# Kernel tuning notes

Measured on AMD Instinct MI355X. Metric: run time of the kernel, lower is better.

## Reference

```python
import jax, jax.numpy as jnp
import numpy as np

K = 256           # number of selected features (init kwarg k)
NUM_SAMPLES = 8   # init kwarg num_samples
BATCH = 256
NUM_FEATURES = 20000


def setup_inputs() -> dict:
    key = jax.random.key(0)
    logits = jax.random.normal(key, (BATCH, NUM_FEATURES, 1), dtype=jnp.float32)
    return {"logits": logits, "tau": 1, "training": 0}


def reference(logits, tau, training):
    # Eval branch of SubsetLayer.forward (training=False).
    # logits: [B, N, 1]
    B, N, _ = logits.shape
    scores = logits[..., 0]                       # [B, N]
    _, idx = jax.lax.top_k(scores, K)             # idx: [B, K]
    # k-hot mask built directly by scatter (equivalent to one_hot(...).sum(1))
    khot = jnp.zeros((B, N), dtype=jnp.float32)
    khot = khot.at[jnp.arange(B)[:, None], idx].set(1.0)  # [B, N]
    # unsqueeze(0).unsqueeze(-1).expand(num_samples, -1, -1, -1)
    out = jnp.broadcast_to(khot[None, :, :, None], (NUM_SAMPLES, B, N, 1))
    return out
```

## Files before the change

### kernel.cpp

```cpp
#include <hip/hip_runtime.h>

#define BATCH   256
#define NFEAT   20000
#define NVEC    (NFEAT / 4)
#define KSEL    256
#define NSAMP   8
#define CAP     2048

typedef unsigned long long u64;
typedef float __attribute__((ext_vector_type(4))) f32x4;

__device__ __forceinline__ unsigned fmap(float f) {
    unsigned u = __float_as_uint(f);
    return (u & 0x80000000u) ? ~u : (u | 0x80000000u);
}

__device__ __forceinline__ void select_bin_wave0(const unsigned* hist, int nbins, int w,
                                                 int* s_d, int* s_w, int lane) {
    for (int base = nbins - 1; base >= 0; base -= 64) {
        int bin = base - lane;
        unsigned c = (bin >= 0) ? hist[bin] : 0u;
        unsigned p = c;
#pragma unroll
        for (int off = 1; off < 64; off <<= 1) {
            unsigned t = __shfl_up(p, off);
            if (lane >= off) p += t;
        }
        unsigned long long m = __ballot(p >= (unsigned)w);
        if (m) {
            int l = __ffsll(m) - 1;
            if (lane == l) { *s_d = bin; *s_w = w - (int)(p - c); }
            return;
        }
        w -= (int)__shfl(p, 63);
    }
    if (lane == 0) { *s_d = 0; *s_w = 1; }
}

__device__ __forceinline__ void pick64(const unsigned* arr, int w, int lane,
                                       int* s_idx, int* s_w) {
    unsigned c = arr[63 - lane];
    unsigned p = c;
#pragma unroll
    for (int off = 1; off < 64; off <<= 1) {
        unsigned t = __shfl_up(p, off);
        if (lane >= off) p += t;
    }
    unsigned long long m = __ballot(p >= (unsigned)w);
    if (m) {
        int l = __ffsll(m) - 1;
        if (lane == l) { *s_idx = 63 - l; *s_w = w - (int)(p - c); }
    } else if (lane == 0) { *s_idx = 0; *s_w = 1; }
}

__global__ __launch_bounds__(1024) void topk_fused(const float* __restrict__ logits,
                                                   float* __restrict__ out) {
    const int b = blockIdx.x, tid = threadIdx.x;
    const int lane = tid & 63, wave = tid >> 6;
    const float4* __restrict__ row4 = (const float4*)(logits + (size_t)b * NFEAT);

    __shared__ unsigned hist[4096];
    __shared__ u64 cand[CAP];
    __shared__ unsigned csum[64];
    __shared__ int s_d, s_w;
    __shared__ unsigned s_cnt;
    __shared__ u64 s_thr;
    __shared__ int s_run, s_cut, s_wc[16];

    float4 v[5];
#pragma unroll
    for (int j = 0; j < 5; ++j) {
        const int i4 = tid + j * 1024;
        v[j] = row4[(i4 < NVEC) ? i4 : (NVEC - 1)];
    }
#pragma unroll
    for (int j = 0; j < 4; ++j) hist[tid + j * 1024] = 0;
    __syncthreads();

    unsigned kk[5][4];
#pragma unroll
    for (int j = 0; j < 5; ++j) {
        kk[j][0] = fmap(v[j].x); kk[j][1] = fmap(v[j].y);
        kk[j][2] = fmap(v[j].z); kk[j][3] = fmap(v[j].w);
    }
#pragma unroll
    for (int j = 0; j < 4; ++j) {
#pragma unroll
        for (int e = 0; e < 4; ++e) atomicAdd(&hist[kk[j][e] >> 20], 1u);
    }
    if (tid + 4096 < NVEC) {
#pragma unroll
        for (int e = 0; e < 4; ++e) atomicAdd(&hist[kk[4][e] >> 20], 1u);
    }
    __syncthreads();

    unsigned keypref; int w;
    {
#pragma unroll
        for (int j = 0; j < 4; ++j) {
            const int c = wave * 4 + j;
            unsigned x = hist[c * 64 + lane];
#pragma unroll
            for (int off = 32; off; off >>= 1) x += __shfl_down(x, off);
            if (lane == 0) csum[c] = x;
        }
        __syncthreads();
        if (wave == 0) pick64(csum, KSEL, lane, &s_d, &s_w);
        __syncthreads();
        const int chunk = s_d; const int w0 = s_w;
        if (wave == 0) pick64(&hist[chunk * 64], w0, lane, &s_d, &s_w);
        if (tid == 0) s_cnt = 0;
        __syncthreads();
        keypref = (unsigned)(chunk * 64 + s_d);
        w = s_w;
    }
    int shift = 20;

    unsigned C;
    for (;;) {
#pragma unroll
        for (int j = 0; j < 5; ++j) {
            const int i4 = tid + j * 1024;
            if (i4 < NVEC) {
#pragma unroll
                for (int e = 0; e < 4; ++e) {
                    const unsigned k = kk[j][e];
                    if ((k >> shift) == keypref) {
                        unsigned p = atomicAdd(&s_cnt, 1u);
                        if (p < CAP) cand[p] = ((u64)k << 32) | (unsigned)~(4 * i4 + e);
                    }
                }
            }
        }
        __syncthreads();
        C = s_cnt;
        if (C <= CAP || shift == 0) break;

        const int nb = (shift >= 12) ? 12 : shift;
        const int nsh = shift - nb;
        for (int i = tid; i < (1 << nb); i += 1024) hist[i] = 0;
        __syncthreads();
#pragma unroll
        for (int j = 0; j < 5; ++j) {
            const int i4 = tid + j * 1024;
            if (i4 < NVEC) {
#pragma unroll
                for (int e = 0; e < 4; ++e) {
                    const unsigned k = kk[j][e];
                    if ((k >> shift) == keypref)
                        atomicAdd(&hist[(k >> nsh) & ((1u << nb) - 1u)], 1u);
                }
            }
        }
        __syncthreads();
        if (wave == 0) select_bin_wave0(hist, 1 << nb, w, &s_d, &s_w, lane);
        if (tid == 0) s_cnt = 0;
        __syncthreads();
        keypref = (keypref << nb) | (unsigned)s_d;
        w = s_w;
        shift = nsh;
    }

    if (C <= CAP) {
        for (int i = tid; i < (int)C; i += 1024) {
            const u64 ci = cand[i];
            int cgt = 0;
            for (int j = 0; j < (int)C; ++j) cgt += (cand[j] > ci) ? 1 : 0;
            if (cgt == w - 1) s_thr = ci;
        }
        __syncthreads();
    } else {
        if (tid == 0) { s_run = 0; s_cut = 0; }
        __syncthreads();
#pragma unroll 1
        for (int j = 0; j < 5; ++j) {
            const int i4 = tid + j * 1024;
            bool eq[4];
            int cnt4 = 0;
#pragma unroll
            for (int e = 0; e < 4; ++e) {
                eq[e] = (i4 < NVEC) && (kk[j][e] == keypref);
                cnt4 += eq[e] ? 1 : 0;
            }
            unsigned p = (unsigned)cnt4;
#pragma unroll
            for (int off = 1; off < 64; off <<= 1) {
                unsigned t = __shfl_up(p, off);
                if (lane >= off) p += t;
            }
            const unsigned excl = p - (unsigned)cnt4;
            if (lane == 63) s_wc[wave] = (int)p;
            __syncthreads();
            int off0 = s_run + (int)excl;
            for (int x = 0; x < wave; ++x) off0 += s_wc[x];
#pragma unroll
            for (int e = 0; e < 4; ++e) {
                if (eq[e]) { if (off0 == w - 1) s_cut = 4 * i4 + e; ++off0; }
            }
            __syncthreads();
            if (tid == 0) { int t = 0; for (int x = 0; x < 16; ++x) t += s_wc[x]; s_run += t; }
            __syncthreads();
            if (s_run >= w) break;
        }
        if (tid == 0) s_thr = ((u64)keypref << 32) | (unsigned)~s_cut;
        __syncthreads();
    }

    const u64 thr = s_thr;
    const unsigned thr_k = (unsigned)(thr >> 32);
    const unsigned thr_l = (unsigned)thr;
    float* const outb = out + (size_t)b * NFEAT;
#pragma unroll
    for (int j = 0; j < 5; ++j) {
        const int i4 = tid + j * 1024;
        if (i4 < NVEC) {
            const int n = 4 * i4;
            f32x4 m;
#pragma unroll
            for (int e = 0; e < 4; ++e) {
                const unsigned k = kk[j][e];
                const bool sel = (k > thr_k) || (k == thr_k && (unsigned)~(n + e) >= thr_l);
                m[e] = sel ? 1.0f : 0.0f;
            }
#pragma unroll
            for (int s = 0; s < NSAMP; ++s) {
                *reinterpret_cast<f32x4*>(outb + (size_t)s * ((size_t)BATCH * NFEAT) + n) = m;
            }
        }
    }
}

extern "C" void kernel_launch(void* const* d_in, const int* in_sizes, int n_in,
                              void* d_out, int out_size, void* d_ws, size_t ws_size,
                              hipStream_t stream) {
    const float* logits = (const float*)d_in[0];
    float* out = (float*)d_out;
    (void)d_ws; (void)ws_size;

    topk_fused<<<BATCH, 1024, 0, stream>>>(logits, out);
}
```

Measured before the change: 36.63 us.

## Overlap zero-fill output stores with top-k selection; write only selected ones

Writes zeros to every output slot early, spread across the histogram and selection phases, so the large output write overlaps the selection compute. At the end it stores 1.0 as scalar writes only for the selected elements, after waiting for the zero stores to finish so the two writes to the same address are ordered. It also replaces __syncthreads with a custom barrier that waits only on LDS counters, so the in-flight global stores do not stall each barrier. The risks are correctness, since ordering relies on the vmcnt wait before the selected-element stores, and scattered scalar stores for the ones.

```diff
diff --git a/kernel.cpp b/kernel.cpp
--- a/kernel.cpp
+++ b/kernel.cpp
@@ -10,6 +10,10 @@
 typedef unsigned long long u64;
 typedef float __attribute__((ext_vector_type(4))) f32x4;
 
+#define BAR() do { asm volatile("s_waitcnt lgkmcnt(0)" ::: "memory"); \
+                   __builtin_amdgcn_s_barrier();                      \
+                   asm volatile("" ::: "memory"); } while (0)
+
 __device__ __forceinline__ unsigned fmap(float f) {
     unsigned u = __float_as_uint(f);
     return (u & 0x80000000u) ? ~u : (u | 0x80000000u);
@@ -58,6 +62,19 @@
     const int b = blockIdx.x, tid = threadIdx.x;
     const int lane = tid & 63, wave = tid >> 6;
     const float4* __restrict__ row4 = (const float4*)(logits + (size_t)b * NFEAT);
+    const size_t BN = (size_t)BATCH * NFEAT;
+    float* const outb = out + (size_t)b * NFEAT;
+    const f32x4 z4 = {0.0f, 0.0f, 0.0f, 0.0f};
+
+#define ZSTORE(J)                                                              \
+    do {                                                                       \
+        const int i4_ = tid + (J) * 1024;                                      \
+        if (i4_ < NVEC) {                                                      \
+            _Pragma("unroll")                                                  \
+            for (int s_ = 0; s_ < NSAMP; ++s_)                                 \
+                *reinterpret_cast<f32x4*>(outb + (size_t)s_ * BN + 4 * i4_) = z4; \
+        }                                                                      \
+    } while (0)
 
     __shared__ unsigned hist[4096];
     __shared__ u64 cand[CAP];
@@ -73,9 +90,11 @@
         const int i4 = tid + j * 1024;
         v[j] = row4[(i4 < NVEC) ? i4 : (NVEC - 1)];
     }
+    ZSTORE(0);
+    ZSTORE(1);
 #pragma unroll
     for (int j = 0; j < 4; ++j) hist[tid + j * 1024] = 0;
-    __syncthreads();
+    BAR();
 
     unsigned kk[5][4];
 #pragma unroll
@@ -92,7 +111,8 @@
 #pragma unroll
         for (int e = 0; e < 4; ++e) atomicAdd(&hist[kk[4][e] >> 20], 1u);
     }
-    __syncthreads();
+    ZSTORE(2);
+    BAR();
 
     unsigned keypref; int w;
     {
@@ -104,17 +124,18 @@
             for (int off = 32; off; off >>= 1) x += __shfl_down(x, off);
             if (lane == 0) csum[c] = x;
         }
-        __syncthreads();
+        BAR();
         if (wave == 0) pick64(csum, KSEL, lane, &s_d, &s_w);
-        __syncthreads();
+        BAR();
         const int chunk = s_d; const int w0 = s_w;
         if (wave == 0) pick64(&hist[chunk * 64], w0, lane, &s_d, &s_w);
         if (tid == 0) s_cnt = 0;
-        __syncthreads();
+        BAR();
         keypref = (unsigned)(chunk * 64 + s_d);
         w = s_w;
     }
     int shift = 20;
+    ZSTORE(3);
 
     unsigned C;
     for (;;) {
@@ -132,14 +153,14 @@
                 }
             }
         }
-        __syncthreads();
+        BAR();
         C = s_cnt;
         if (C <= CAP || shift == 0) break;
 
         const int nb = (shift >= 12) ? 12 : shift;
         const int nsh = shift - nb;
         for (int i = tid; i < (1 << nb); i += 1024) hist[i] = 0;
-        __syncthreads();
+        BAR();
 #pragma unroll
         for (int j = 0; j < 5; ++j) {
             const int i4 = tid + j * 1024;
@@ -152,14 +173,15 @@
                 }
             }
         }
-        __syncthreads();
+        BAR();
         if (wave == 0) select_bin_wave0(hist, 1 << nb, w, &s_d, &s_w, lane);
         if (tid == 0) s_cnt = 0;
-        __syncthreads();
+        BAR();
         keypref = (keypref << nb) | (unsigned)s_d;
         w = s_w;
         shift = nsh;
     }
+    ZSTORE(4);
 
     if (C <= CAP) {
         for (int i = tid; i < (int)C; i += 1024) {
@@ -168,10 +190,10 @@
             for (int j = 0; j < (int)C; ++j) cgt += (cand[j] > ci) ? 1 : 0;
             if (cgt == w - 1) s_thr = ci;
         }
-        __syncthreads();
+        BAR();
     } else {
         if (tid == 0) { s_run = 0; s_cut = 0; }
-        __syncthreads();
+        BAR();
 #pragma unroll 1
         for (int j = 0; j < 5; ++j) {
             const int i4 = tid + j * 1024;
@@ -190,44 +212,44 @@
             }
             const unsigned excl = p - (unsigned)cnt4;
             if (lane == 63) s_wc[wave] = (int)p;
-            __syncthreads();
+            BAR();
             int off0 = s_run + (int)excl;
             for (int x = 0; x < wave; ++x) off0 += s_wc[x];
 #pragma unroll
             for (int e = 0; e < 4; ++e) {
                 if (eq[e]) { if (off0 == w - 1) s_cut = 4 * i4 + e; ++off0; }
             }
-            __syncthreads();
+            BAR();
             if (tid == 0) { int t = 0; for (int x = 0; x < 16; ++x) t += s_wc[x]; s_run += t; }
-            __syncthreads();
+            BAR();
             if (s_run >= w) break;
         }
         if (tid == 0) s_thr = ((u64)keypref << 32) | (unsigned)~s_cut;
-        __syncthreads();
+        BAR();
     }
 
     const u64 thr = s_thr;
     const unsigned thr_k = (unsigned)(thr >> 32);
     const unsigned thr_l = (unsigned)thr;
-    float* const outb = out + (size_t)b * NFEAT;
+    asm volatile("s_waitcnt vmcnt(0)" ::: "memory");
 #pragma unroll
     for (int j = 0; j < 5; ++j) {
         const int i4 = tid + j * 1024;
         if (i4 < NVEC) {
             const int n = 4 * i4;
-            f32x4 m;
 #pragma unroll
             for (int e = 0; e < 4; ++e) {
                 const unsigned k = kk[j][e];
                 const bool sel = (k > thr_k) || (k == thr_k && (unsigned)~(n + e) >= thr_l);
-                m[e] = sel ? 1.0f : 0.0f;
-            }
-#pragma unroll
-            for (int s = 0; s < NSAMP; ++s) {
-                *reinterpret_cast<f32x4*>(outb + (size_t)s * ((size_t)BATCH * NFEAT) + n) = m;
-            }
-        }
-    }
+                if (sel) {
+#pragma unroll
+                    for (int s = 0; s < NSAMP; ++s)
+                        outb[(size_t)s * BN + n + e] = 1.0f;
+                }
+            }
+        }
+    }
+#undef ZSTORE
 }
 
 extern "C" void kernel_launch(void* const* d_in, const int* in_sizes, int n_in,
```

After: 34.64 us. 1.06x faster.

## Split top-k threshold selection from output writing into a separate wide-grid kernel

Applied to the files above, without the earlier changes.

The fused kernel is split in two. The first computes a per-row threshold key and stores it in workspace. A second, wide-grid kernel rereads the logits, recomputes the mask and writes all eight sample copies. The aim is to spread the large output write over many small blocks instead of 256 large ones. In exchange it pays for an extra kernel launch and a second read of the logits.

```diff
diff --git a/kernel.cpp b/kernel.cpp
--- a/kernel.cpp
+++ b/kernel.cpp
@@ -53,8 +53,8 @@
     } else if (lane == 0) { *s_idx = 0; *s_w = 1; }
 }
 
-__global__ __launch_bounds__(1024) void topk_fused(const float* __restrict__ logits,
-                                                   float* __restrict__ out) {
+__global__ __launch_bounds__(1024) void topk_select(const float* __restrict__ logits,
+                                                    u64* __restrict__ rowthr) {
     const int b = blockIdx.x, tid = threadIdx.x;
     const int lane = tid & 63, wave = tid >> 6;
     const float4* __restrict__ row4 = (const float4*)(logits + (size_t)b * NFEAT);
@@ -206,27 +206,36 @@
         __syncthreads();
     }
 
-    const u64 thr = s_thr;
+    if (tid == 0) rowthr[b] = s_thr;
+}
+
+__global__ __launch_bounds__(256) void write_out(const float* __restrict__ logits,
+                                                 const u64* __restrict__ rowthr,
+                                                 float* __restrict__ out) {
+    const int b = blockIdx.y;
+    const int q = blockIdx.x * 256 + threadIdx.x;
+    if (q >= NVEC) return;
+
+    const u64 thr = rowthr[b];
     const unsigned thr_k = (unsigned)(thr >> 32);
     const unsigned thr_l = (unsigned)thr;
-    float* const outb = out + (size_t)b * NFEAT;
-#pragma unroll
-    for (int j = 0; j < 5; ++j) {
-        const int i4 = tid + j * 1024;
-        if (i4 < NVEC) {
-            const int n = 4 * i4;
-            f32x4 m;
-#pragma unroll
-            for (int e = 0; e < 4; ++e) {
-                const unsigned k = kk[j][e];
-                const bool sel = (k > thr_k) || (k == thr_k && (unsigned)~(n + e) >= thr_l);
-                m[e] = sel ? 1.0f : 0.0f;
-            }
-#pragma unroll
-            for (int s = 0; s < NSAMP; ++s) {
-                *reinterpret_cast<f32x4*>(outb + (size_t)s * ((size_t)BATCH * NFEAT) + n) = m;
-            }
-        }
+    const int n = q * 4;
+    const float4 v = *reinterpret_cast<const float4*>(logits + (size_t)b * NFEAT + n);
+
+    f32x4 m;
+    {
+        const float* vf = &v.x;
+#pragma unroll
+        for (int j = 0; j < 4; ++j) {
+            const unsigned k = fmap(vf[j]);
+            const bool sel = (k > thr_k) || (k == thr_k && (unsigned)~(n + j) >= thr_l);
+            m[j] = sel ? 1.0f : 0.0f;
+        }
+    }
+
+#pragma unroll
+    for (int s = 0; s < NSAMP; ++s) {
+        *reinterpret_cast<f32x4*>(out + ((size_t)s * BATCH + b) * NFEAT + n) = m;
     }
 }
 
@@ -235,7 +244,10 @@
                               hipStream_t stream) {
     const float* logits = (const float*)d_in[0];
     float* out = (float*)d_out;
-    (void)d_ws; (void)ws_size;
-
-    topk_fused<<<BATCH, 1024, 0, stream>>>(logits, out);
-}
+    u64* rowthr = (u64*)d_ws;
+
+    topk_select<<<BATCH, 1024, 0, stream>>>(logits, rowthr);
+
+    dim3 grid((NVEC + 255) / 256, BATCH);
+    write_out<<<grid, 256, 0, stream>>>(logits, rowthr, out);
+}
```

New measurement: 41.38 us. 1.13x slower.
